# Performance work log

Measured on AMD Instinct MI355X. Metric: run time of the kernel, lower is better.

## Reference

```python
import jax, jax.numpy as jnp
import numpy as np

B, H, S, D = 1, 16, 4096, 64

def setup_inputs() -> dict:
    key = jax.random.key(0)
    kq, kk, kv = jax.random.split(key, 3)
    q = jax.random.normal(kq, (B, H, S, D), dtype=jnp.float32)
    k = jax.random.normal(kk, (B, H, S, D), dtype=jnp.float32)
    v = jax.random.normal(kv, (B, H, S, D), dtype=jnp.float32)
    # causal mask, broadcastable over batch and heads: True = attend
    mask = jnp.tril(jnp.ones((S, S), dtype=bool))[None, None, :, :]
    return {"q": q, "k": k, "v": v, "mask": mask}


def reference(q, k, v, mask):
    # Chunked attention in the original is mathematically identical to full
    # attention: each query-chunk softmaxes over ALL keys. Vectorized form:
    dim_head = q.shape[-1]
    scale = 1.0 / jnp.sqrt(jnp.asarray(dim_head, dtype=q.dtype))
    scores = jnp.einsum("bhqd,bhkd->bhqk", q, k) * scale  # [B,H,S,S]
    scores = jnp.where(mask, scores, -jnp.inf)
    attn = jax.nn.softmax(scores, axis=-1)
    attn = jnp.nan_to_num(attn, nan=0.0)  # rows with all keys masked -> 0
    return jnp.einsum("bhqk,bhkd->bhqd", attn, v)
```

## Files before the change

kernel.cpp:

```cpp
#include <hip/hip_runtime.h>
#include <hip/hip_bf16.h>
#include <math.h>


typedef __bf16 bf16;
typedef __bf16 bf16x8 __attribute__((ext_vector_type(8)));
typedef float f32x16 __attribute__((ext_vector_type(16)));

#define NH 16
#define SEQ 4096
#define DH 64
#define QB 128
#define WQ 32
#define KB 128
#define LOG2E 1.44269504088896340736f

#define NSLOT 512
#define WS_O 256
#define O_BYTES (NSLOT * 128 * 64 * 2)
#define WS_M (WS_O + O_BYTES)
#define WS_L (WS_M + NSLOT * 128 * 4)
#define WS_NEED (WS_L + NSLOT * 128 * 4)

static __device__ __forceinline__ void mfma32(f32x16& c, bf16x8 a, bf16x8 b) {
  asm("v_mfma_f32_32x32x16_bf16 %0, %1, %2, %0" : "+v"(c) : "v"(a), "v"(b));
}
static __device__ __forceinline__ float exp2a(float x) {
  float r; asm("v_exp_f32 %0, %1" : "=v"(r) : "v"(x)); return r;
}
static __device__ __forceinline__ unsigned pk(float lo, float hi) {
  unsigned r; asm("v_cvt_pk_bf16_f32 %0, %1, %2" : "=v"(r) : "v"(lo), "v"(hi)); return r;
}
static __device__ __forceinline__ void swap32(unsigned& a, unsigned& b) {
  asm("v_permlane32_swap_b32 %0, %1" : "+v"(a), "+v"(b));
}

union AFrag { unsigned u[4]; bf16x8 v; };

static __device__ __forceinline__ bf16x8 cvt8(float4 a, float4 b) {
  bf16x8 f;
  f[0]=(bf16)a.x; f[1]=(bf16)a.y; f[2]=(bf16)a.z; f[3]=(bf16)a.w;
  f[4]=(bf16)b.x; f[5]=(bf16)b.y; f[6]=(bf16)b.z; f[7]=(bf16)b.w;
  return f;
}

__global__ void zero_ctr(unsigned* c) { if (threadIdx.x == 0) *c = 0; }

__global__ __launch_bounds__(256, 2)
void fa_fwd(const float* __restrict__ Q, const float* __restrict__ K,
            const float* __restrict__ V, float* __restrict__ O,
            void* __restrict__ ws, const int nitems, const int split) {
  __shared__ bf16 Ksh[2][KB * DH];
  __shared__ bf16 Vts[2][DH * KB];
  __shared__ int sh_item;

  unsigned* ctr = (unsigned*)ws;

  const int tid = threadIdx.x;
  const int w   = tid >> 6;
  const int l   = tid & 63;
  const int lc  = l & 31;
  const int hi  = l >> 5;

  const int kr = tid >> 1, kc = (tid & 1) * 32;
  const int dg = tid & 7,  kp2 = tid >> 3;

  for (;;) {
    __syncthreads();
    if (tid == 0) sh_item = (int)atomicAdd(ctr, 1u);
    __syncthreads();
    const int c = sh_item;
    if (c >= nitems) break;

    int head, qb, t0, t1, slot = -1;
    if (!split) {
      head = c & 15; const int qblk = 31 - (c >> 4);
      qb = qblk * QB; t0 = 0; t1 = qblk + 1;
    } else if (c < 256) {
      head = c & 15; const int qblk = 16 + (c >> 4);
      qb = qblk * QB; t0 = 0; t1 = 16;
      slot = ((head << 4) + (qblk - 16)) * 2;
    } else if (c < 512) {
      const int i = c - 256; head = i & 15; const int qblk = 31 - (i >> 4);
      qb = qblk * QB; t0 = 16; t1 = qblk + 1;
      slot = ((head << 4) + (qblk - 16)) * 2 + 1;
    } else {
      const int i = c - 512; head = i & 15; const int qblk = 15 - (i >> 4);
      qb = qblk * QB; t0 = 0; t1 = qblk + 1;
    }

    const int qw = qb + w * WQ;
    const int qv = qw + lc;
    const float* Qh = Q + (size_t)head * SEQ * DH;
    const float* Kh = K + (size_t)head * SEQ * DH;
    const float* Vh = V + (size_t)head * SEQ * DH;

    bf16x8 qf[4];
    {
      const float* qp = Qh + (size_t)qv * DH + hi * 8;
      const float sc = 0.125f * LOG2E;
#pragma unroll
      for (int ch = 0; ch < 4; ++ch) {
        float4 x = *(const float4*)(qp + ch * 16);
        float4 y = *(const float4*)(qp + ch * 16 + 4);
        bf16x8 f;
        f[0]=(bf16)(x.x*sc); f[1]=(bf16)(x.y*sc); f[2]=(bf16)(x.z*sc); f[3]=(bf16)(x.w*sc);
        f[4]=(bf16)(y.x*sc); f[5]=(bf16)(y.y*sc); f[6]=(bf16)(y.z*sc); f[7]=(bf16)(y.w*sc);
        qf[ch] = f;
      }
    }

    f32x16 o0 = {}, o1 = {};
    float m = -INFINITY, ls = 0.f;

    float4 kreg[8], vreg[8];
    {
      const int kb0 = t0 * KB;
      const float* p = Kh + (size_t)(kb0 + kr) * DH + kc;
#pragma unroll
      for (int i = 0; i < 8; ++i) kreg[i] = ((const float4*)p)[i];
#pragma unroll
      for (int u = 0; u < 2; ++u) {
        const float* pv = Vh + (size_t)(kb0 + 2 * (kp2 + 32 * u)) * DH + dg * 8;
        vreg[u*4+0] = ((const float4*)pv)[0];
        vreg[u*4+1] = ((const float4*)pv)[1];
        vreg[u*4+2] = ((const float4*)(pv + DH))[0];
        vreg[u*4+3] = ((const float4*)(pv + DH))[1];
      }
    }

    for (int t = t0; t < t1; ++t) {
      const int kb = t * KB;
      const int b  = (t - t0) & 1;

      {
        const int Sk = (((kr & 7) ^ ((kr >> 3) & 7)) << 4);
#pragma unroll
        for (int q = 0; q < 4; ++q)
          *(bf16x8*)((char*)Ksh[b] + kr * 128 + ((kc * 2 + q * 16) ^ Sk)) =
              cvt8(kreg[2*q], kreg[2*q+1]);
        const int xbase = (kp2 * 4) ^ (dg << 4);
#pragma unroll
        for (int u = 0; u < 2; ++u) {
          const int xb = xbase + u * 128;
#pragma unroll
          for (int i = 0; i < 8; ++i) {
            const float lo = vreg[u*4 + (i >> 2)    ][i & 3];
            const float hv = vreg[u*4 + (i >> 2) + 2][i & 3];
            *(unsigned*)((char*)Vts[b] + (dg * 8 + i) * 256 + (xb ^ (i << 4))) =
                pk(lo, hv);
          }
        }
      }
      __syncthreads();

      if (t + 1 < t1) {
        const int kn = kb + KB;
        const float* p = Kh + (size_t)(kn + kr) * DH + kc;
#pragma unroll
        for (int i = 0; i < 8; ++i) kreg[i] = ((const float4*)p)[i];
#pragma unroll
        for (int u = 0; u < 2; ++u) {
          const float* pv = Vh + (size_t)(kn + 2 * (kp2 + 32 * u)) * DH + dg * 8;
          vreg[u*4+0] = ((const float4*)pv)[0];
          vreg[u*4+1] = ((const float4*)pv)[1];
          vreg[u*4+2] = ((const float4*)(pv + DH))[0];
          vreg[u*4+3] = ((const float4*)(pv + DH))[1];
        }
      }

#pragma unroll
      for (int hb = 0; hb < 2; ++hb) {
        if (kb + hb * 64 > qw + 31) continue;

        f32x16 st0 = {}, st1 = {};
#pragma unroll
        for (int kt = 0; kt < 2; ++kt) {
          const int row = hb * 64 + kt * 32;
          const int Sr  = (((lc & 7) ^ ((kt * 4 + (lc >> 3)) & 7)) << 4);
          f32x16& st = kt ? st1 : st0;
#pragma unroll
          for (int ch = 0; ch < 4; ++ch) {
            const bf16x8 kf = *(const bf16x8*)((const char*)Ksh[b] +
                (row + lc) * 128 + ((ch * 32 + hi * 16) ^ Sr));
            mfma32(st, kf, qf[ch]);
          }
        }

        if (kb + hb * 64 + 63 > qw) {
#pragma unroll
          for (int r = 0; r < 16; ++r) {
            const int kg = kb + hb * 64 + ((r & 3) + 8 * (r >> 2) + 4 * hi);
            if (kg > qv)      st0[r] = -INFINITY;
            if (kg + 32 > qv) st1[r] = -INFINITY;
          }
        }

        float acc[8];
#pragma unroll
        for (int i = 0; i < 8; ++i)
          acc[i] = fmaxf(fmaxf(st0[i], st0[i + 8]), fmaxf(st1[i], st1[i + 8]));
        acc[0]=fmaxf(acc[0],acc[4]); acc[1]=fmaxf(acc[1],acc[5]);
        acc[2]=fmaxf(acc[2],acc[6]); acc[3]=fmaxf(acc[3],acc[7]);
        acc[0]=fmaxf(acc[0],acc[2]); acc[1]=fmaxf(acc[1],acc[3]);
        float mx = fmaxf(acc[0], acc[1]);
        mx = fmaxf(mx, __shfl_xor(mx, 32));

        if (__any(mx > m + 8.0f)) {
          const float mn = fmaxf(m, mx);
          const float al = exp2a(m - mn);
          m = mn;
          ls *= al;
#pragma unroll
          for (int r = 0; r < 16; ++r) {
            const float aq = __shfl(al, (r & 3) + 8 * (r >> 2) + 4 * hi);
            o0[r] *= aq; o1[r] *= aq;
          }
        }

        float rs = 0.f;
#pragma unroll
        for (int ks = 0; ks < 4; ++ks) {
          const f32x16& st = (ks < 2) ? st0 : st1;
          float p[8];
#pragma unroll
          for (int j = 0; j < 8; ++j) p[j] = exp2a(st[(ks & 1) * 8 + j] - m);
          rs += ((p[0]+p[1])+(p[2]+p[3])) + ((p[4]+p[5])+(p[6]+p[7]));
          unsigned u0 = pk(p[0],p[1]), u1 = pk(p[2],p[3]);
          unsigned u2 = pk(p[4],p[5]), u3 = pk(p[6],p[7]);
          swap32(u0, u2); swap32(u1, u3);
          AFrag af; af.u[0]=u0; af.u[1]=u1; af.u[2]=u2; af.u[3]=u3;
          const int koff = hb * 128 + ks * 32 + hi * 16;
          const int S0 = (((lc & 7) ^ ((lc >> 3) & 7)) << 4);
          const int S1 = (((lc & 7) ^ (((lc >> 3) + 4) & 7)) << 4);
          bf16x8 v0 = *(const bf16x8*)((const char*)Vts[b] + lc * 256 + (koff ^ S0));
          bf16x8 v1 = *(const bf16x8*)((const char*)Vts[b] + (lc + 32) * 256 + (koff ^ S1));
          mfma32(o0, af.v, v0);
          mfma32(o1, af.v, v1);
        }
        rs += __shfl_xor(rs, 32);
        ls += rs;
      }

      if (t + 1 < t1) __syncthreads();
    }

    if (slot < 0) {
      const float inv = 1.0f / ls;
      float* Ob = O + (size_t)(head * SEQ + qw) * DH;
#pragma unroll
      for (int r = 0; r < 16; ++r) {
        const int row = (r & 3) + 8 * (r >> 2) + 4 * hi;
        const float iq = __shfl(inv, row);
        Ob[(size_t)row * DH + lc]      = o0[r] * iq;
        Ob[(size_t)row * DH + 32 + lc] = o1[r] * iq;
      }
    } else {
      bf16* po = (bf16*)((char*)ws + WS_O) + (size_t)slot * (128 * 64);
#pragma unroll
      for (int r = 0; r < 16; ++r) {
        const int row = w * WQ + (r & 3) + 8 * (r >> 2) + 4 * hi;
        po[row * 64 + lc]      = (bf16)o0[r];
        po[row * 64 + 32 + lc] = (bf16)o1[r];
      }
      if (hi == 0) {
        ((float*)((char*)ws + WS_M))[slot * 128 + w * WQ + lc] = m;
        ((float*)((char*)ws + WS_L))[slot * 128 + w * WQ + lc] = ls;
      }
    }
  }
}

__global__ __launch_bounds__(256)
void fa_combine(float* __restrict__ O, const void* __restrict__ ws) {
  const int idx   = blockIdx.x * 256 + threadIdx.x;
  const int dpart = idx & 7;
  const int row8  = idx >> 3;
  const int r     = row8 & 127;
  const int qb16  = (row8 >> 7) & 15;
  const int h     = row8 >> 11;
  const int s0    = ((h << 4) + qb16) * 2;

  const float* pm = (const float*)((const char*)ws + WS_M);
  const float* pl = (const float*)((const char*)ws + WS_L);
  const float m0 = pm[s0 * 128 + r], m1 = pm[(s0 + 1) * 128 + r];
  const float l0 = pl[s0 * 128 + r], l1 = pl[(s0 + 1) * 128 + r];
  const float M  = fmaxf(m0, m1);
  const float w0 = exp2f(m0 - M), w1 = exp2f(m1 - M);
  const float inv = 1.0f / (l0 * w0 + l1 * w1);

  const bf16* po = (const bf16*)((const char*)ws + WS_O);
  const bf16x8 a = *(const bf16x8*)(po + (size_t)s0 * 8192 + r * 64 + dpart * 8);
  const bf16x8 b = *(const bf16x8*)(po + (size_t)(s0 + 1) * 8192 + r * 64 + dpart * 8);

  float* out = O + ((size_t)h * SEQ + (16 + qb16) * 128 + r) * DH + dpart * 8;
#pragma unroll
  for (int j = 0; j < 8; ++j)
    out[j] = ((float)a[j] * w0 + (float)b[j] * w1) * inv;
}

extern "C" void kernel_launch(void* const* d_in, const int* in_sizes, int n_in,
                              void* d_out, int out_size, void* d_ws, size_t ws_size,
                              hipStream_t stream) {
  const float* q = (const float*)d_in[0];
  const float* k = (const float*)d_in[1];
  const float* v = (const float*)d_in[2];
  float* out = (float*)d_out;
  const int split = (ws_size >= (size_t)WS_NEED) ? 1 : 0;

  zero_ctr<<<1, 64, 0, stream>>>((unsigned*)d_ws);
  fa_fwd<<<512, 256, 0, stream>>>(q, k, v, out, d_ws, split ? 768 : 512, split);
  if (split) fa_combine<<<1024, 256, 0, stream>>>(out, d_ws);
}
```

Before: 211.7 us.

## Halve KV tile, raise occupancy, and split more query blocks adaptively

Shrinks the K/V tile from 128 to 64 rows, which halves shared memory and register staging, and raises launch bounds to 4 blocks per CU with twice as many persistent blocks. Query blocks with index at or above a workspace-dependent threshold (8, 16 or 32) are now split into two halves over the key range, with a combine kernel merging the partial results. The intent is better load balance and more latency hiding across the causal workload. The cost is more loop iterations and barriers per tile, plus extra workspace traffic and combine work for the split blocks.

```diff
diff --git a/kernel.cpp b/kernel.cpp
--- a/kernel.cpp
+++ b/kernel.cpp
@@ -12,15 +12,11 @@
 #define DH 64
 #define QB 128
 #define WQ 32
-#define KB 128
+#define KB 64
 #define LOG2E 1.44269504088896340736f
 
-#define NSLOT 512
-#define WS_O 256
-#define O_BYTES (NSLOT * 128 * 64 * 2)
-#define WS_M (WS_O + O_BYTES)
-#define WS_L (WS_M + NSLOT * 128 * 4)
-#define WS_NEED (WS_L + NSLOT * 128 * 4)
+#define NEED8  13369600ull
+#define NEED16 8913152ull
 
 static __device__ __forceinline__ void mfma32(f32x16& c, bf16x8 a, bf16x8 b) {
   asm("v_mfma_f32_32x32x16_bf16 %0, %1, %2, %0" : "+v"(c) : "v"(a), "v"(b));
@@ -46,15 +42,20 @@
 
 __global__ void zero_ctr(unsigned* c) { if (threadIdx.x == 0) *c = 0; }
 
-__global__ __launch_bounds__(256, 2)
+__global__ __launch_bounds__(256, 4)
 void fa_fwd(const float* __restrict__ Q, const float* __restrict__ K,
             const float* __restrict__ V, float* __restrict__ O,
-            void* __restrict__ ws, const int nitems, const int split) {
+            void* __restrict__ ws, const int nitems, const int s) {
   __shared__ bf16 Ksh[2][KB * DH];
   __shared__ bf16 Vts[2][DH * KB];
   __shared__ int sh_item;
 
   unsigned* ctr = (unsigned*)ws;
+  const int ns    = 32 - s;
+  const int nslot = 32 * ns;
+  bf16*  wsO = (bf16*)((char*)ws + 256);
+  float* wsM = (float*)((char*)ws + 256 + (size_t)nslot * 16384);
+  float* wsL = wsM + (size_t)nslot * 128;
 
   const int tid = threadIdx.x;
   const int w   = tid >> 6;
@@ -62,8 +63,8 @@
   const int lc  = l & 31;
   const int hi  = l >> 5;
 
-  const int kr = tid >> 1, kc = (tid & 1) * 32;
-  const int dg = tid & 7,  kp2 = tid >> 3;
+  const int kr = tid >> 2, kc = (tid & 3) * 16;
+  const int dg = tid & 7,  kp = tid >> 3;
 
   for (;;) {
     __syncthreads();
@@ -73,20 +74,19 @@
     if (c >= nitems) break;
 
     int head, qb, t0, t1, slot = -1;
-    if (!split) {
-      head = c & 15; const int qblk = 31 - (c >> 4);
-      qb = qblk * QB; t0 = 0; t1 = qblk + 1;
-    } else if (c < 256) {
-      head = c & 15; const int qblk = 16 + (c >> 4);
-      qb = qblk * QB; t0 = 0; t1 = 16;
-      slot = ((head << 4) + (qblk - 16)) * 2;
-    } else if (c < 512) {
-      const int i = c - 256; head = i & 15; const int qblk = 31 - (i >> 4);
-      qb = qblk * QB; t0 = 16; t1 = qblk + 1;
-      slot = ((head << 4) + (qblk - 16)) * 2 + 1;
+    if (c < ns * 16) {
+      head = c & 15; const int j = 31 - (c >> 4);
+      qb = j * QB; t0 = 0; t1 = j + 1;
+      slot = ((j - s) * 16 + head) * 2;
+    } else if (c < 2 * ns * 16) {
+      const int i = c - ns * 16;
+      head = i & 15; const int j = 31 - (i >> 4);
+      qb = j * QB; t0 = j + 1; t1 = 2 * j + 2;
+      slot = ((j - s) * 16 + head) * 2 + 1;
     } else {
-      const int i = c - 512; head = i & 15; const int qblk = 15 - (i >> 4);
-      qb = qblk * QB; t0 = 0; t1 = qblk + 1;
+      const int i = c - 2 * ns * 16;
+      head = i & 15; const int j = (s - 1) - (i >> 4);
+      qb = j * QB; t0 = 0; t1 = 2 * j + 2;
     }
 
     const int qw = qb + w * WQ;
@@ -113,20 +113,17 @@
     f32x16 o0 = {}, o1 = {};
     float m = -INFINITY, ls = 0.f;
 
-    float4 kreg[8], vreg[8];
+    float4 kreg[4], vreg[4];
     {
       const int kb0 = t0 * KB;
       const float* p = Kh + (size_t)(kb0 + kr) * DH + kc;
 #pragma unroll
-      for (int i = 0; i < 8; ++i) kreg[i] = ((const float4*)p)[i];
-#pragma unroll
-      for (int u = 0; u < 2; ++u) {
-        const float* pv = Vh + (size_t)(kb0 + 2 * (kp2 + 32 * u)) * DH + dg * 8;
-        vreg[u*4+0] = ((const float4*)pv)[0];
-        vreg[u*4+1] = ((const float4*)pv)[1];
-        vreg[u*4+2] = ((const float4*)(pv + DH))[0];
-        vreg[u*4+3] = ((const float4*)(pv + DH))[1];
-      }
+      for (int i = 0; i < 4; ++i) kreg[i] = ((const float4*)p)[i];
+      const float* pv = Vh + (size_t)(kb0 + 2 * kp) * DH + dg * 8;
+      vreg[0] = ((const float4*)pv)[0];
+      vreg[1] = ((const float4*)pv)[1];
+      vreg[2] = ((const float4*)(pv + DH))[0];
+      vreg[3] = ((const float4*)(pv + DH))[1];
     }
 
     for (int t = t0; t < t1; ++t) {
@@ -136,20 +133,16 @@
       {
         const int Sk = (((kr & 7) ^ ((kr >> 3) & 7)) << 4);
 #pragma unroll
-        for (int q = 0; q < 4; ++q)
+        for (int q = 0; q < 2; ++q)
           *(bf16x8*)((char*)Ksh[b] + kr * 128 + ((kc * 2 + q * 16) ^ Sk)) =
               cvt8(kreg[2*q], kreg[2*q+1]);
-        const int xbase = (kp2 * 4) ^ (dg << 4);
-#pragma unroll
-        for (int u = 0; u < 2; ++u) {
-          const int xb = xbase + u * 128;
-#pragma unroll
-          for (int i = 0; i < 8; ++i) {
-            const float lo = vreg[u*4 + (i >> 2)    ][i & 3];
-            const float hv = vreg[u*4 + (i >> 2) + 2][i & 3];
-            *(unsigned*)((char*)Vts[b] + (dg * 8 + i) * 256 + (xb ^ (i << 4))) =
-                pk(lo, hv);
-          }
+        const int xbase = (kp * 4) ^ (dg << 4);
+#pragma unroll
+        for (int i = 0; i < 8; ++i) {
+          const float lo = vreg[(i >> 2)    ][i & 3];
+          const float hv = vreg[(i >> 2) + 2][i & 3];
+          *(unsigned*)((char*)Vts[b] + (dg * 8 + i) * 128 + (xbase ^ (i << 4))) =
+              pk(lo, hv);
         }
       }
       __syncthreads();
@@ -158,91 +151,83 @@
         const int kn = kb + KB;
         const float* p = Kh + (size_t)(kn + kr) * DH + kc;
 #pragma unroll
-        for (int i = 0; i < 8; ++i) kreg[i] = ((const float4*)p)[i];
-#pragma unroll
-        for (int u = 0; u < 2; ++u) {
-          const float* pv = Vh + (size_t)(kn + 2 * (kp2 + 32 * u)) * DH + dg * 8;
-          vreg[u*4+0] = ((const float4*)pv)[0];
-          vreg[u*4+1] = ((const float4*)pv)[1];
-          vreg[u*4+2] = ((const float4*)(pv + DH))[0];
-          vreg[u*4+3] = ((const float4*)(pv + DH))[1];
+        for (int i = 0; i < 4; ++i) kreg[i] = ((const float4*)p)[i];
+        const float* pv = Vh + (size_t)(kn + 2 * kp) * DH + dg * 8;
+        vreg[0] = ((const float4*)pv)[0];
+        vreg[1] = ((const float4*)pv)[1];
+        vreg[2] = ((const float4*)(pv + DH))[0];
+        vreg[3] = ((const float4*)(pv + DH))[1];
+      }
+
+      if (kb > qw + 31) continue;
+
+      f32x16 st0 = {}, st1 = {};
+#pragma unroll
+      for (int kt = 0; kt < 2; ++kt) {
+        const int row = kt * 32 + lc;
+        const int Sr  = (((lc & 7) ^ ((kt * 4 + (lc >> 3)) & 7)) << 4);
+        f32x16& st = kt ? st1 : st0;
+#pragma unroll
+        for (int ch = 0; ch < 4; ++ch) {
+          const bf16x8 kf = *(const bf16x8*)((const char*)Ksh[b] +
+              row * 128 + ((ch * 32 + hi * 16) ^ Sr));
+          mfma32(st, kf, qf[ch]);
         }
       }
 
-#pragma unroll
-      for (int hb = 0; hb < 2; ++hb) {
-        if (kb + hb * 64 > qw + 31) continue;
-
-        f32x16 st0 = {}, st1 = {};
-#pragma unroll
-        for (int kt = 0; kt < 2; ++kt) {
-          const int row = hb * 64 + kt * 32;
-          const int Sr  = (((lc & 7) ^ ((kt * 4 + (lc >> 3)) & 7)) << 4);
-          f32x16& st = kt ? st1 : st0;
-#pragma unroll
-          for (int ch = 0; ch < 4; ++ch) {
-            const bf16x8 kf = *(const bf16x8*)((const char*)Ksh[b] +
-                (row + lc) * 128 + ((ch * 32 + hi * 16) ^ Sr));
-            mfma32(st, kf, qf[ch]);
-          }
+      if (kb + 63 > qw) {
+#pragma unroll
+        for (int r = 0; r < 16; ++r) {
+          const int kg = kb + ((r & 3) + 8 * (r >> 2) + 4 * hi);
+          if (kg > qv)      st0[r] = -INFINITY;
+          if (kg + 32 > qv) st1[r] = -INFINITY;
         }
-
-        if (kb + hb * 64 + 63 > qw) {
-#pragma unroll
-          for (int r = 0; r < 16; ++r) {
-            const int kg = kb + hb * 64 + ((r & 3) + 8 * (r >> 2) + 4 * hi);
-            if (kg > qv)      st0[r] = -INFINITY;
-            if (kg + 32 > qv) st1[r] = -INFINITY;
-          }
+      }
+
+      float acc[8];
+#pragma unroll
+      for (int i = 0; i < 8; ++i)
+        acc[i] = fmaxf(fmaxf(st0[i], st0[i + 8]), fmaxf(st1[i], st1[i + 8]));
+      acc[0]=fmaxf(acc[0],acc[4]); acc[1]=fmaxf(acc[1],acc[5]);
+      acc[2]=fmaxf(acc[2],acc[6]); acc[3]=fmaxf(acc[3],acc[7]);
+      acc[0]=fmaxf(acc[0],acc[2]); acc[1]=fmaxf(acc[1],acc[3]);
+      float mx = fmaxf(acc[0], acc[1]);
+      mx = fmaxf(mx, __shfl_xor(mx, 32));
+
+      if (__any(mx > m + 8.0f)) {
+        const float mn = fmaxf(m, mx);
+        const float al = exp2a(m - mn);
+        m = mn;
+        ls *= al;
+#pragma unroll
+        for (int r = 0; r < 16; ++r) {
+          const float aq = __shfl(al, (r & 3) + 8 * (r >> 2) + 4 * hi);
+          o0[r] *= aq; o1[r] *= aq;
         }
-
-        float acc[8];
-#pragma unroll
-        for (int i = 0; i < 8; ++i)
-          acc[i] = fmaxf(fmaxf(st0[i], st0[i + 8]), fmaxf(st1[i], st1[i + 8]));
-        acc[0]=fmaxf(acc[0],acc[4]); acc[1]=fmaxf(acc[1],acc[5]);
-        acc[2]=fmaxf(acc[2],acc[6]); acc[3]=fmaxf(acc[3],acc[7]);
-        acc[0]=fmaxf(acc[0],acc[2]); acc[1]=fmaxf(acc[1],acc[3]);
-        float mx = fmaxf(acc[0], acc[1]);
-        mx = fmaxf(mx, __shfl_xor(mx, 32));
-
-        if (__any(mx > m + 8.0f)) {
-          const float mn = fmaxf(m, mx);
-          const float al = exp2a(m - mn);
-          m = mn;
-          ls *= al;
-#pragma unroll
-          for (int r = 0; r < 16; ++r) {
-            const float aq = __shfl(al, (r & 3) + 8 * (r >> 2) + 4 * hi);
-            o0[r] *= aq; o1[r] *= aq;
-          }
-        }
-
-        float rs = 0.f;
-#pragma unroll
-        for (int ks = 0; ks < 4; ++ks) {
-          const f32x16& st = (ks < 2) ? st0 : st1;
-          float p[8];
-#pragma unroll
-          for (int j = 0; j < 8; ++j) p[j] = exp2a(st[(ks & 1) * 8 + j] - m);
-          rs += ((p[0]+p[1])+(p[2]+p[3])) + ((p[4]+p[5])+(p[6]+p[7]));
-          unsigned u0 = pk(p[0],p[1]), u1 = pk(p[2],p[3]);
-          unsigned u2 = pk(p[4],p[5]), u3 = pk(p[6],p[7]);
-          swap32(u0, u2); swap32(u1, u3);
-          AFrag af; af.u[0]=u0; af.u[1]=u1; af.u[2]=u2; af.u[3]=u3;
-          const int koff = hb * 128 + ks * 32 + hi * 16;
-          const int S0 = (((lc & 7) ^ ((lc >> 3) & 7)) << 4);
-          const int S1 = (((lc & 7) ^ (((lc >> 3) + 4) & 7)) << 4);
-          bf16x8 v0 = *(const bf16x8*)((const char*)Vts[b] + lc * 256 + (koff ^ S0));
-          bf16x8 v1 = *(const bf16x8*)((const char*)Vts[b] + (lc + 32) * 256 + (koff ^ S1));
-          mfma32(o0, af.v, v0);
-          mfma32(o1, af.v, v1);
-        }
-        rs += __shfl_xor(rs, 32);
-        ls += rs;
-      }
-
-      if (t + 1 < t1) __syncthreads();
+      }
+
+      float rs = 0.f;
+      const int S0 = (((lc & 7) ^ ((lc >> 3) & 7)) << 4);
+      const int S1 = (((lc & 7) ^ (((lc >> 3) + 4) & 7)) << 4);
+#pragma unroll
+      for (int ks = 0; ks < 4; ++ks) {
+        const f32x16& st = (ks < 2) ? st0 : st1;
+        float p[8];
+#pragma unroll
+        for (int j = 0; j < 8; ++j) p[j] = exp2a(st[(ks & 1) * 8 + j] - m);
+        rs += ((p[0]+p[1])+(p[2]+p[3])) + ((p[4]+p[5])+(p[6]+p[7]));
+        unsigned u0 = pk(p[0],p[1]), u1 = pk(p[2],p[3]);
+        unsigned u2 = pk(p[4],p[5]), u3 = pk(p[6],p[7]);
+        swap32(u0, u2); swap32(u1, u3);
+        AFrag af; af.u[0]=u0; af.u[1]=u1; af.u[2]=u2; af.u[3]=u3;
+        const int koff = ks * 32 + hi * 16;
+        bf16x8 v0 = *(const bf16x8*)((const char*)Vts[b] + lc * 128 + (koff ^ S0));
+        bf16x8 v1 = *(const bf16x8*)((const char*)Vts[b] + (lc + 32) * 128 + (koff ^ S1));
+        mfma32(o0, af.v, v0);
+        mfma32(o1, af.v, v1);
+      }
+      rs += __shfl_xor(rs, 32);
+      ls += rs;
     }
 
     if (slot < 0) {
@@ -256,7 +241,7 @@
         Ob[(size_t)row * DH + 32 + lc] = o1[r] * iq;
       }
     } else {
-      bf16* po = (bf16*)((char*)ws + WS_O) + (size_t)slot * (128 * 64);
+      bf16* po = wsO + (size_t)slot * (128 * 64);
 #pragma unroll
       for (int r = 0; r < 16; ++r) {
         const int row = w * WQ + (r & 3) + 8 * (r >> 2) + 4 * hi;
@@ -264,36 +249,38 @@
         po[row * 64 + 32 + lc] = (bf16)o1[r];
       }
       if (hi == 0) {
-        ((float*)((char*)ws + WS_M))[slot * 128 + w * WQ + lc] = m;
-        ((float*)((char*)ws + WS_L))[slot * 128 + w * WQ + lc] = ls;
+        wsM[slot * 128 + w * WQ + lc] = m;
+        wsL[slot * 128 + w * WQ + lc] = ls;
       }
     }
   }
 }
 
 __global__ __launch_bounds__(256)
-void fa_combine(float* __restrict__ O, const void* __restrict__ ws) {
-  const int idx   = blockIdx.x * 256 + threadIdx.x;
-  const int dpart = idx & 7;
-  const int row8  = idx >> 3;
-  const int r     = row8 & 127;
-  const int qb16  = (row8 >> 7) & 15;
-  const int h     = row8 >> 11;
-  const int s0    = ((h << 4) + qb16) * 2;
-
-  const float* pm = (const float*)((const char*)ws + WS_M);
-  const float* pl = (const float*)((const char*)ws + WS_L);
-  const float m0 = pm[s0 * 128 + r], m1 = pm[(s0 + 1) * 128 + r];
-  const float l0 = pl[s0 * 128 + r], l1 = pl[(s0 + 1) * 128 + r];
+void fa_combine(float* __restrict__ O, const void* __restrict__ ws, const int s) {
+  const int ns    = 32 - s;
+  const int nslot = 32 * ns;
+  const bf16*  wsO = (const bf16*)((const char*)ws + 256);
+  const float* wsM = (const float*)((const char*)ws + 256 + (size_t)nslot * 16384);
+  const float* wsL = wsM + (size_t)nslot * 128;
+
+  const int li    = blockIdx.x * 256 + threadIdx.x;
+  const int dpart = li & 7;
+  const int r     = li >> 3;
+  const int jj    = blockIdx.y;
+  const int h     = blockIdx.z;
+  const int s0    = (jj * 16 + h) * 2;
+
+  const float m0 = wsM[s0 * 128 + r], m1 = wsM[(s0 + 1) * 128 + r];
+  const float l0 = wsL[s0 * 128 + r], l1 = wsL[(s0 + 1) * 128 + r];
   const float M  = fmaxf(m0, m1);
   const float w0 = exp2f(m0 - M), w1 = exp2f(m1 - M);
   const float inv = 1.0f / (l0 * w0 + l1 * w1);
 
-  const bf16* po = (const bf16*)((const char*)ws + WS_O);
-  const bf16x8 a = *(const bf16x8*)(po + (size_t)s0 * 8192 + r * 64 + dpart * 8);
-  const bf16x8 b = *(const bf16x8*)(po + (size_t)(s0 + 1) * 8192 + r * 64 + dpart * 8);
-
-  float* out = O + ((size_t)h * SEQ + (16 + qb16) * 128 + r) * DH + dpart * 8;
+  const bf16x8 a = *(const bf16x8*)(wsO + (size_t)s0 * 8192 + r * 64 + dpart * 8);
+  const bf16x8 b = *(const bf16x8*)(wsO + (size_t)(s0 + 1) * 8192 + r * 64 + dpart * 8);
+
+  float* out = O + ((size_t)h * SEQ + (s + jj) * 128 + r) * DH + dpart * 8;
 #pragma unroll
   for (int j = 0; j < 8; ++j)
     out[j] = ((float)a[j] * w0 + (float)b[j] * w1) * inv;
@@ -306,9 +293,15 @@
   const float* k = (const float*)d_in[1];
   const float* v = (const float*)d_in[2];
   float* out = (float*)d_out;
-  const int split = (ws_size >= (size_t)WS_NEED) ? 1 : 0;
+
+  int s;
+  if      (ws_size >= NEED8)  s = 8;
+  else if (ws_size >= NEED16) s = 16;
+  else                        s = 32;
+  const int ns = 32 - s;
+  const int nitems = 2 * ns * 16 + s * 16;
 
   zero_ctr<<<1, 64, 0, stream>>>((unsigned*)d_ws);
-  fa_fwd<<<512, 256, 0, stream>>>(q, k, v, out, d_ws, split ? 768 : 512, split);
-  if (split) fa_combine<<<1024, 256, 0, stream>>>(out, d_ws);
-}
+  fa_fwd<<<1024, 256, 0, stream>>>(q, k, v, out, d_ws, nitems, s);
+  if (ns > 0) fa_combine<<<dim3(4, ns, 16), 256, 0, stream>>>(out, d_ws, s);
+}
```

Result: slower. 357.5 us (+68.8%).
